# Performance work log

Measured on AMD Instinct MI355X. Metric: run time of the kernel, lower is better.

## Reference

```python
import jax, jax.numpy as jnp
import numpy as np

N_NODES = 100000
N_EDGES = 1600000
NUM_GRAPHS = 64
IN_CH, HID, NUM_CLASSES = 128, 64, 10


def _glorot(key, fan_in, fan_out):
    scale = jnp.sqrt(2.0 / (fan_in + fan_out)).astype(jnp.float32)
    return jax.random.normal(key, (fan_in, fan_out), jnp.float32) * scale


def setup_inputs() -> dict:
    key = jax.random.key(0)
    ks = jax.random.split(key, 7)
    x = jax.random.normal(ks[0], (N_NODES, IN_CH), jnp.float32)
    edge_index = jax.random.randint(ks[1], (2, N_EDGES), 0, N_NODES, dtype=jnp.int32)
    batch = jnp.sort(jax.random.randint(ks[2], (N_NODES,), 0, NUM_GRAPHS, dtype=jnp.int32))
    return {
        "x": x,
        "edge_index": edge_index,
        "batch": batch,
        "W1": _glorot(ks[3], IN_CH, HID), "b1": jnp.zeros((HID,), jnp.float32),
        "W2": _glorot(ks[4], HID, HID), "b2": jnp.zeros((HID,), jnp.float32),
        "W3": _glorot(ks[5], HID, NUM_CLASSES), "b3": jnp.zeros((NUM_CLASSES,), jnp.float32),
    }


def _gcn_conv(x, src, dst, norm, W, b):
    # GCNConv: h = X W, then symmetric-normalized scatter-add over edges, then + b
    h = x @ W                                  # [N, out]
    msg = norm[:, None] * h[src]               # [E+N, out] gather
    out = jax.ops.segment_sum(msg, dst, num_segments=N_NODES)
    return out + b


def reference(x, edge_index, batch, W1, b1, W2, b2, W3, b3):
    loop = jnp.arange(N_NODES, dtype=edge_index.dtype)
    src = jnp.concatenate([edge_index[0], loop])   # self-loops added (PyG gcn_norm)
    dst = jnp.concatenate([edge_index[1], loop])
    deg = jax.ops.segment_sum(jnp.ones(src.shape[0], x.dtype), dst, num_segments=N_NODES)
    dinv = jnp.where(deg > 0, jax.lax.rsqrt(deg), jnp.zeros_like(deg))
    norm = dinv[src] * dinv[dst]

    h = jax.nn.relu(_gcn_conv(x, src, dst, norm, W1, b1))  # dropout is identity in eval
    h = jax.nn.relu(_gcn_conv(h, src, dst, norm, W2, b2))
    h = _gcn_conv(h, src, dst, norm, W3, b3)

    counts = jax.ops.segment_sum(jnp.ones(N_NODES, h.dtype), batch, num_segments=NUM_GRAPHS)
    pooled = jax.ops.segment_sum(h, batch, num_segments=NUM_GRAPHS) / jnp.maximum(counts, 1.0)[:, None]
    return jax.nn.log_softmax(pooled, axis=1)
```

## Files before the change

kernel.cpp:

```cpp
#include <hip/hip_runtime.h>
#include <math.h>

#define IN_CH 128
#define HID   64
#define NC    10
#define BSH   8
#define NBLK  256

typedef unsigned short bfu;
typedef __attribute__((ext_vector_type(8))) short bf16x8;
typedef __attribute__((ext_vector_type(4))) float f32x4;
typedef __attribute__((ext_vector_type(2))) float f32x2;

static __device__ __forceinline__ bfu bf16_of(float f) {
    unsigned u = __float_as_uint(f);
    unsigned r = (u + 0x7FFF + ((u >> 16) & 1)) >> 16;
    return (bfu)r;
}

#if __has_builtin(__builtin_amdgcn_cvt_pk_f32_fp8) && __has_builtin(__builtin_amdgcn_cvt_pk_fp8_f32)
template <bool HI>
static __device__ __forceinline__ f32x2 fp8_unpk(unsigned d) {
    return __builtin_amdgcn_cvt_pk_f32_fp8((int)d, HI);
}
template <bool HI>
static __device__ __forceinline__ int fp8_pk(float a, float b, int old) {
    return __builtin_amdgcn_cvt_pk_fp8_f32(a, b, old, HI);
}
#else
static __device__ __forceinline__ float fp8_dec1(unsigned b) {
    unsigned s = b >> 7, e = (b >> 3) & 15, m = b & 7;
    float v = (e == 0) ? ldexpf((float)m, -9) : ldexpf((float)(8 + m), (int)e - 10);
    return s ? -v : v;
}
static __device__ __forceinline__ unsigned fp8_enc1(float f) {
    unsigned u = __float_as_uint(f);
    unsigned s = (u >> 31) << 7;
    f = fabsf(f);
    if (!(f < 448.f)) return s | 0x7E;
    if (f < 0.015625f) {
        int q = (int)rintf(f * 512.f);
        return s | (unsigned)q;
    }
    int e; float fr = frexpf(f, &e);
    int q = (int)rintf(fr * 16.f);
    if (q == 16) { q = 8; e++; }
    int E = e + 6;
    if (E >= 16) return s | 0x7E;
    return s | (unsigned)((E << 3) | (q - 8));
}
template <bool HI>
static __device__ __forceinline__ f32x2 fp8_unpk(unsigned d) {
    unsigned w = HI ? (d >> 16) : d;
    f32x2 r; r.x = fp8_dec1(w & 0xFF); r.y = fp8_dec1((w >> 8) & 0xFF);
    return r;
}
template <bool HI>
static __device__ __forceinline__ int fp8_pk(float a, float b, int old) {
    unsigned p = fp8_enc1(a) | (fp8_enc1(b) << 8);
    return HI ? (int)(((unsigned)old & 0x0000FFFFu) | (p << 16))
              : (int)(((unsigned)old & 0xFFFF0000u) | p);
}
#endif

__device__ __forceinline__ int lower_bound_i(const int* a, int n, int v) {
    int lo = 0, hi = n;
    while (lo < hi) { int mid = (lo + hi) >> 1; if (a[mid] < v) lo = mid + 1; else hi = mid; }
    return lo;
}


__global__ void k_init(int* __restrict__ cnt, float* __restrict__ Psum,
                       unsigned* __restrict__ dumA, unsigned* __restrict__ dumB,
                       int nbuck, int ng) {
    int t = threadIdx.x;
    for (int i = t; i < nbuck; i += 512) cnt[i] = 0;
    for (int i = t; i < ng * HID; i += 512) Psum[i] = 0.f;
    if (t < 16) { dumA[t] = 0u; dumB[t] = 0u; }
}


__global__ __launch_bounds__(1024) void k_part(const int* __restrict__ src,
                                               const int* __restrict__ dst,
                                               int* __restrict__ cnt,
                                               unsigned* __restrict__ packed,
                                               int E, int nbuck, int chunk, int cap) {
    __shared__ int hist[512];
    int tid = threadIdx.x;
    for (int b = tid; b < nbuck; b += 1024) hist[b] = 0;
    __syncthreads();
    int base = blockIdx.x * chunk;
    int lim  = min(base + chunk, E);
    for (int e = base + tid; e < lim; e += 1024)
        atomicAdd(&hist[dst[e] >> BSH], 1);
    __syncthreads();
    for (int b = tid; b < nbuck; b += 1024) {
        int c = hist[b];
        hist[b] = c ? atomicAdd(&cnt[b], c) : 0;
    }
    __syncthreads();
    for (int e = base + tid; e < lim; e += 1024) {
        int d = dst[e], s = src[e];
        int b = d >> BSH;
        int pos = atomicAdd(&hist[b], 1);
        if (pos < cap)
            packed[(size_t)b * (size_t)cap + pos] = ((unsigned)s << 8) | (unsigned)(d & 255);
    }
}


__global__ __launch_bounds__(512) void k_placeC(const unsigned* __restrict__ packed,
                                                const int* __restrict__ cnt,
                                                int2* __restrict__ rp2,
                                                float* __restrict__ dinv,
                                                int* __restrict__ meta,
                                                int nn, int cap, int capm) {
    __shared__ int hist[256];
    __shared__ int scn[256];
    __shared__ int cur[256];
    int tid = threadIdx.x;
    int b   = blockIdx.x;
    int nb0 = b << BSH;
    int nnb = min(1 << BSH, nn - nb0);
    if (tid < 256) hist[tid] = 0;
    __syncthreads();
    int lo = b * cap;
    int hi = lo + min(cnt[b], cap);
    for (int e = lo + tid; e < hi; e += blockDim.x)
        atomicAdd(&hist[packed[e] & 255u], 1);
    __syncthreads();
    int pd = 0;
    if (tid < 256) { pd = (hist[tid] + 3) & ~3; scn[tid] = pd; }
    __syncthreads();
    for (int off = 1; off < 256; off <<= 1) {
        int t = 0;
        if (tid < 256 && tid >= off) t = scn[tid - off];
        __syncthreads();
        if (tid < 256) scn[tid] += t;
        __syncthreads();
    }
    int meta0 = b * capm;
    if (tid < nnb) {
        int rp = meta0 + scn[tid] - pd;
        rp2[nb0 + tid] = make_int2(rp, rp + pd);
        cur[tid] = rp;
        dinv[nb0 + tid] = rsqrtf((float)(hist[tid] + 1));
        for (int k = hist[tid]; k < pd; k++) meta[rp + k] = nn;
    }
    __syncthreads();
    for (int e = lo + tid; e < hi; e += blockDim.x) {
        unsigned p = packed[e];
        int pos = atomicAdd(&cur[p & 255u], 1);
        meta[pos] = (int)(p >> 8);
    }
}


template <int K, bool IN_BF16>
__global__ __launch_bounds__(256) void k_gemm(const void* __restrict__ Xv,
                                              const float* __restrict__ W,
                                              const float* __restrict__ dinv,
                                              unsigned char* __restrict__ G8, int n) {
    constexpr int KS = K + 8;
    __shared__ bfu wt[64 * KS];
    int tid = threadIdx.x;
    for (int i = tid; i < K * 64; i += 256) {
        int k = i >> 6, nn2 = i & 63;
        wt[nn2 * KS + k] = bf16_of(W[i]);
    }
    __syncthreads();
    int wave = tid >> 6, lane = tid & 63;
    int m = lane & 15, q = lane >> 4;
    int row0 = blockIdx.x * 64 + wave * 16;
    int rowA = min(row0 + m, n - 1);
    f32x4 acc[4] = {{0.f,0.f,0.f,0.f},{0.f,0.f,0.f,0.f},
                    {0.f,0.f,0.f,0.f},{0.f,0.f,0.f,0.f}};
#pragma unroll
    for (int ks = 0; ks < K / 32; ks++) {
        bf16x8 a;
        if (IN_BF16) {
            a = *(const bf16x8*)((const bfu*)Xv + (size_t)rowA * 64 + ks * 32 + q * 8);
        } else {
            const float* xp = (const float*)Xv + (size_t)rowA * K + ks * 32 + q * 8;
            float4 v0 = *(const float4*)xp;
            float4 v1 = *(const float4*)(xp + 4);
            union { unsigned u[4]; bf16x8 v; } cvt;
            cvt.u[0] = __builtin_amdgcn_perm(__float_as_uint(v0.y), __float_as_uint(v0.x), 0x07060302u);
            cvt.u[1] = __builtin_amdgcn_perm(__float_as_uint(v0.w), __float_as_uint(v0.z), 0x07060302u);
            cvt.u[2] = __builtin_amdgcn_perm(__float_as_uint(v1.y), __float_as_uint(v1.x), 0x07060302u);
            cvt.u[3] = __builtin_amdgcn_perm(__float_as_uint(v1.w), __float_as_uint(v1.z), 0x07060302u);
            a = cvt.v;
        }
#pragma unroll
        for (int nt = 0; nt < 4; nt++) {
            bf16x8 b = *(const bf16x8*)&wt[(nt * 16 + m) * KS + ks * 32 + q * 8];
            acc[nt] = __builtin_amdgcn_mfma_f32_16x16x32_bf16(a, b, acc[nt], 0, 0, 0);
        }
    }
#pragma unroll
    for (int r = 0; r < 4; r++) {
        int grow = row0 + q * 4 + r;
        if (grow < n) {
            float dv = dinv[grow];
            int p01 = fp8_pk<false>(acc[0][r] * dv, acc[1][r] * dv, 0);
            int p23 = fp8_pk<false>(acc[2][r] * dv, acc[3][r] * dv, 0);
            unsigned char* gp = G8 + (size_t)grow * 64 + m;
            gp[0]  = (unsigned char)(p01 & 0xFF);
            gp[16] = (unsigned char)((p01 >> 8) & 0xFF);
            gp[32] = (unsigned char)(p23 & 0xFF);
            gp[48] = (unsigned char)((p23 >> 8) & 0xFF);
        }
    }
}


template <int MODE>
__global__ void k_agg(const unsigned* __restrict__ G4, const int* __restrict__ meta,
                      const int2* __restrict__ rp2, const float* __restrict__ dinv,
                      const float* __restrict__ bias, void* __restrict__ outv,
                      const int* __restrict__ batch, float* __restrict__ Psum,
                      const float* __restrict__ Wg,
                      int n, int ng, int do_relu, int post_scale) {
    extern __shared__ char smem[];
    int tid = threadIdx.x;
    if (MODE == 3) {
        bfu* wt = (bfu*)(smem + 16 * 72 * 2);
        for (int i = tid; i < 64 * 64; i += 256) {
            int k = i >> 6, c = i & 63;
            wt[c * 72 + k] = bf16_of(Wg[i]);
        }
    }
    int wbase = ((blockIdx.x * blockDim.x + tid) >> 6) * 4;
    if (MODE == 1) { if (wbase >= n) return; }
    int lane = tid & 63;
    int col4 = lane & 15, equad = lane >> 4;
    int nb0 = blockIdx.x * 16;
    if (MODE == 2 && tid < 16) {
        int* sb = (int*)(smem + 16 * 64 * 4);
        sb[tid] = (nb0 + tid < n) ? batch[nb0 + tid] : -1;
    }
    int nd    = wbase + equad;
    bool alive = nd < n;
    int ndc   = alive ? nd : (n - 1);
    int2 rp = rp2[ndc];
    int beg = rp.x, pend = alive ? rp.y : rp.x;
    f32x2 aA = {0.f, 0.f}, aB = {0.f, 0.f};
    for (int e = beg; e < pend; e += 4) {
        int4 m = *(const int4*)&meta[e];
        unsigned d0 = G4[(size_t)m.x * 16 + col4];
        unsigned d1 = G4[(size_t)m.y * 16 + col4];
        unsigned d2 = G4[(size_t)m.z * 16 + col4];
        unsigned d3 = G4[(size_t)m.w * 16 + col4];
        aA += fp8_unpk<false>(d0); aB += fp8_unpk<true>(d0);
        aA += fp8_unpk<false>(d1); aB += fp8_unpk<true>(d1);
        aA += fp8_unpk<false>(d2); aB += fp8_unpk<true>(d2);
        aA += fp8_unpk<false>(d3); aB += fp8_unpk<true>(d3);
    }
    unsigned sv = G4[(size_t)ndc * 16 + col4];
    aA += fp8_unpk<false>(sv); aB += fp8_unpk<true>(sv);
    float dv = dinv[ndc];
    float a0 = aA.x * dv, a1 = aA.y * dv, a2 = aB.x * dv, a3 = aB.y * dv;
    if (bias) {
        float4 bv = *(const float4*)&bias[col4 * 4];
        a0 += bv.x; a1 += bv.y; a2 += bv.z; a3 += bv.w;
    }
    if (do_relu) {
        a0 = fmaxf(a0, 0.f); a1 = fmaxf(a1, 0.f);
        a2 = fmaxf(a2, 0.f); a3 = fmaxf(a3, 0.f);
    }
    if (post_scale) { a0 *= dv; a1 *= dv; a2 *= dv; a3 *= dv; }
    if (MODE == 3) {
        bfu* pw = (bfu*)smem;
        bfu* wt = (bfu*)(smem + 16 * 72 * 2);
        int slot = (tid >> 6) * 4 + equad;
        uint2 o;
        o.x = (unsigned)bf16_of(alive ? a0 : 0.f) | ((unsigned)bf16_of(alive ? a1 : 0.f) << 16);
        o.y = (unsigned)bf16_of(alive ? a2 : 0.f) | ((unsigned)bf16_of(alive ? a3 : 0.f) << 16);
        *(uint2*)&pw[slot * 72 + col4 * 4] = o;
        __syncthreads();
        int w = tid >> 6, m = col4, q = equad;
        f32x4 acc = {0.f, 0.f, 0.f, 0.f};
#pragma unroll
        for (int ks = 0; ks < 2; ks++) {
            bf16x8 av = *(const bf16x8*)&pw[m * 72 + ks * 32 + q * 8];
            bf16x8 bv = *(const bf16x8*)&wt[(w * 16 + m) * 72 + ks * 32 + q * 8];
            acc = __builtin_amdgcn_mfma_f32_16x16x32_bf16(av, bv, acc, 0, 0, 0);
        }
        int c = w * 16 + m;
        int r0 = nb0 + q * 4;
        float dv0 = dinv[min(r0 + 0, n - 1)], dv1 = dinv[min(r0 + 1, n - 1)];
        float dv2 = dinv[min(r0 + 2, n - 1)], dv3 = dinv[min(r0 + 3, n - 1)];
        int p01 = fp8_pk<false>(acc[0] * dv0, acc[1] * dv1, 0);
        int p23 = fp8_pk<false>(acc[2] * dv2, acc[3] * dv3, 0);
        unsigned char* gp = (unsigned char*)outv;
        if (r0 + 0 < n) gp[(size_t)(r0 + 0) * 64 + c] = (unsigned char)(p01 & 0xFF);
        if (r0 + 1 < n) gp[(size_t)(r0 + 1) * 64 + c] = (unsigned char)((p01 >> 8) & 0xFF);
        if (r0 + 2 < n) gp[(size_t)(r0 + 2) * 64 + c] = (unsigned char)(p23 & 0xFF);
        if (r0 + 3 < n) gp[(size_t)(r0 + 3) * 64 + c] = (unsigned char)((p23 >> 8) & 0xFF);
    } else if (MODE == 2) {
        float* pwf = (float*)smem;
        int*   sb  = (int*)(smem + 16 * 64 * 4);
        int slot = (tid >> 6) * 4 + equad;
        f32x4 st;
        st.x = alive ? a0 : 0.f; st.y = alive ? a1 : 0.f;
        st.z = alive ? a2 : 0.f; st.w = alive ? a3 : 0.f;
        *(f32x4*)&pwf[slot * 64 + col4 * 4] = st;
        __syncthreads();
        int r = tid >> 6, cc = tid & 63;
        int g0 = sb[0];
        float v = 0.f;
#pragma unroll
        for (int s2 = 0; s2 < 16; s2++)
            if (sb[s2] == g0 + r) v += pwf[s2 * 64 + cc];
        if (v != 0.f && g0 + r < ng) atomicAdd(&Psum[(g0 + r) * 64 + cc], v);
        if (tid < 16) {
            int bb = sb[tid];
            if (bb > g0 + 3) {
                for (int c2 = 0; c2 < 64; c2++)
                    atomicAdd(&Psum[bb * 64 + c2], pwf[tid * 64 + c2]);
            }
        }
    } else if (alive) {
        int p = fp8_pk<false>(a0, a1, 0);
        p = fp8_pk<true>(a2, a3, p);
        ((unsigned*)outv)[(size_t)nd * 16 + col4] = (unsigned)p;
    }
}


__global__ void k_final(const float* __restrict__ Psum, const int* __restrict__ batch,
                        int n, const float* __restrict__ W3, const float* __restrict__ b3,
                        float* __restrict__ out, int ng) {
    __shared__ float P[64 * 64];
    __shared__ float s[64][NC];
    __shared__ float lse[64];
    __shared__ float invc[64];
    int t = threadIdx.x;
    if (t < ng) {
        int lo = lower_bound_i(batch, n, t);
        int hi = lower_bound_i(batch, n, t + 1);
        invc[t] = 1.f / (float)max(hi - lo, 1);
    }
    __syncthreads();
    for (int i = t; i < ng * 64; i += blockDim.x) P[i] = Psum[i] * invc[i >> 6];
    __syncthreads();
    if (t < ng * NC) {
        int g = t / NC, c = t % NC;
        float acc = b3[c];
        for (int k = 0; k < 64; k++) acc += P[g * 64 + k] * W3[k * NC + c];
        s[g][c] = acc;
    }
    __syncthreads();
    if (t < ng) {
        float m = -1e30f;
        for (int c = 0; c < NC; c++) m = fmaxf(m, s[t][c]);
        float sum = 0.f;
        for (int c = 0; c < NC; c++) sum += expf(s[t][c] - m);
        lse[t] = m + logf(sum);
    }
    __syncthreads();
    if (t < ng * NC) {
        int g = t / NC, c = t % NC;
        out[t] = s[g][c] - lse[g];
    }
}


extern "C" void kernel_launch(void* const* d_in, const int* in_sizes, int n_in,
                              void* d_out, int out_size, void* d_ws, size_t ws_size,
                              hipStream_t stream) {
    const float* x     = (const float*)d_in[0];
    const int*   ei    = (const int*)  d_in[1];
    const int*   batch = (const int*)  d_in[2];
    const float* W1    = (const float*)d_in[3];
    const float* b1    = (const float*)d_in[4];
    const float* W2    = (const float*)d_in[5];
    const float* b2    = (const float*)d_in[6];
    const float* W3    = (const float*)d_in[7];
    const float* b3    = (const float*)d_in[8];
    float*       out   = (float*)d_out;

    const int NN = in_sizes[0] / IN_CH;
    const int E  = in_sizes[1] / 2;
    const int NG = out_size / NC;
    const int nbuck = (NN + (1 << BSH) - 1) >> BSH;
    const int cap   = (int)(((((long long)E << BSH) / NN) + 768 + 3) & ~3LL);
    const int capm  = cap + 772;

    const int* src = ei;
    const int* dst = ei + E;

    char* ws = (char*)d_ws;
    size_t off = 0;
    auto carve = [&](size_t bytes) -> char* {
        char* p = ws + off;
        off = (off + bytes + 255) & ~(size_t)255;
        return p;
    };
    int2*  rp2    = (int2*) carve((size_t)NN * 8);
    float* dinv   = (float*)carve((size_t)NN * 4);
    int*   cnt    = (int*)  carve((size_t)nbuck * 4);
    int*   meta   = (int*)  carve(((size_t)nbuck * capm + 64) * 4);
    unsigned char* f8A = (unsigned char*)carve((size_t)(NN + 1) * 64);
    unsigned char* f8B = (unsigned char*)carve((size_t)(NN + 1) * 64);
    unsigned* packed = (unsigned*)carve((size_t)nbuck * cap * 4);
    float* Psum   = (float*)carve((size_t)NG * HID * 4);
    (void)ws_size;

    const int chnk = (E + NBLK - 1) / NBLK;
    const int nbG  = (NN + 63) / 64;
    const int nbA  = (NN + 15) / 16;

    const int smem3 = (16 * 72 + 64 * 72) * 2;
    const int smem2 = 16 * 64 * 4 + 16 * 4;

    k_init<<<1, 512, 0, stream>>>(cnt, Psum,
                                  (unsigned*)(f8A + (size_t)NN * 64),
                                  (unsigned*)(f8B + (size_t)NN * 64), nbuck, NG);
    k_part<<<NBLK, 1024, 0, stream>>>(src, dst, cnt, packed, E, nbuck, chnk, cap);
    k_placeC<<<nbuck, 512, 0, stream>>>(packed, cnt, rp2, dinv, meta, NN, cap, capm);

    k_gemm<IN_CH, false><<<nbG, 256, 0, stream>>>(x, W1, dinv, f8A, NN);
    k_agg<3><<<nbA, 256, smem3, stream>>>((const unsigned*)f8A, meta, rp2, dinv, b1,
                                          f8B, nullptr, nullptr, W2, NN, NG, 1, 0);
    k_agg<1><<<nbA, 256, 0, stream>>>((const unsigned*)f8B, meta, rp2, dinv, b2,
                                      f8A, nullptr, nullptr, nullptr, NN, NG, 1, 1);
    k_agg<2><<<nbA, 256, smem2, stream>>>((const unsigned*)f8A, meta, rp2, dinv, nullptr,
                                          nullptr, batch, Psum, nullptr, NN, NG, 0, 0);
    k_final<<<1, 640, 0, stream>>>(Psum, batch, NN, W3, b3, out, NG);
}
```

Before: 246.4 us.

## Pre-convert weights to bf16 once, unroll aggregation gather, widen placement blocks

Weights W1 and W2 are converted to transposed, padded bf16 once in a multi-block init kernel. The GEMM and layer-1 aggregation blocks then copy them into shared memory with 16-byte vector loads instead of each block converting fp32 again. The aggregation inner loop gathers 8 neighbours per iteration, and the self-feature and dinv loads are hoisted ahead of the loop to add memory-level parallelism. k_placeC now launches 1024 threads per block. This adds small workspace buffers and relies on the padded layouts matching the shared-memory strides exactly.

```diff
diff --git a/kernel.cpp b/kernel.cpp
--- a/kernel.cpp
+++ b/kernel.cpp
@@ -72,11 +72,30 @@
 
 __global__ void k_init(int* __restrict__ cnt, float* __restrict__ Psum,
                        unsigned* __restrict__ dumA, unsigned* __restrict__ dumB,
+                       const float* __restrict__ W1, const float* __restrict__ W2,
+                       bfu* __restrict__ W1b, bfu* __restrict__ W2b,
                        int nbuck, int ng) {
-    int t = threadIdx.x;
-    for (int i = t; i < nbuck; i += 512) cnt[i] = 0;
-    for (int i = t; i < ng * HID; i += 512) Psum[i] = 0.f;
-    if (t < 16) { dumA[t] = 0u; dumB[t] = 0u; }
+    int t = threadIdx.x, b = blockIdx.x;
+    if (b == 0) {
+        for (int i = t; i < nbuck; i += 256) cnt[i] = 0;
+        if (t < 16) { dumA[t] = 0u; dumB[t] = 0u; }
+    } else if (b == 1) {
+        for (int i = t; i < ng * HID; i += 256) Psum[i] = 0.f;
+    } else if (b < 6) {
+        int base = (b - 2) * 2048;
+        for (int i = t; i < 2048; i += 256) {
+            int idx = base + i;
+            int k = idx >> 6, c = idx & 63;
+            W1b[c * 136 + k] = bf16_of(W1[idx]);
+        }
+    } else {
+        int base = (b - 6) * 2048;
+        for (int i = t; i < 2048; i += 256) {
+            int idx = base + i;
+            int k = idx >> 6, c = idx & 63;
+            W2b[c * 72 + k] = bf16_of(W2[idx]);
+        }
+    }
 }
 
 
@@ -109,12 +128,12 @@
 }
 
 
-__global__ __launch_bounds__(512) void k_placeC(const unsigned* __restrict__ packed,
-                                                const int* __restrict__ cnt,
-                                                int2* __restrict__ rp2,
-                                                float* __restrict__ dinv,
-                                                int* __restrict__ meta,
-                                                int nn, int cap, int capm) {
+__global__ __launch_bounds__(1024) void k_placeC(const unsigned* __restrict__ packed,
+                                                 const int* __restrict__ cnt,
+                                                 int2* __restrict__ rp2,
+                                                 float* __restrict__ dinv,
+                                                 int* __restrict__ meta,
+                                                 int nn, int cap, int capm) {
     __shared__ int hist[256];
     __shared__ int scn[256];
     __shared__ int cur[256];
@@ -158,15 +177,16 @@
 
 template <int K, bool IN_BF16>
 __global__ __launch_bounds__(256) void k_gemm(const void* __restrict__ Xv,
-                                              const float* __restrict__ W,
+                                              const bfu* __restrict__ Wb,
                                               const float* __restrict__ dinv,
                                               unsigned char* __restrict__ G8, int n) {
     constexpr int KS = K + 8;
     __shared__ bfu wt[64 * KS];
     int tid = threadIdx.x;
-    for (int i = tid; i < K * 64; i += 256) {
-        int k = i >> 6, nn2 = i & 63;
-        wt[nn2 * KS + k] = bf16_of(W[i]);
+    {
+        const uint4* wsrc = (const uint4*)Wb;
+        uint4* wdst = (uint4*)wt;
+        for (int i = tid; i < 8 * KS; i += 256) wdst[i] = wsrc[i];
     }
     __syncthreads();
     int wave = tid >> 6, lane = tid & 63;
@@ -219,16 +239,15 @@
                       const int2* __restrict__ rp2, const float* __restrict__ dinv,
                       const float* __restrict__ bias, void* __restrict__ outv,
                       const int* __restrict__ batch, float* __restrict__ Psum,
-                      const float* __restrict__ Wg,
+                      const bfu* __restrict__ Wb,
                       int n, int ng, int do_relu, int post_scale) {
     extern __shared__ char smem[];
     int tid = threadIdx.x;
     if (MODE == 3) {
         bfu* wt = (bfu*)(smem + 16 * 72 * 2);
-        for (int i = tid; i < 64 * 64; i += 256) {
-            int k = i >> 6, c = i & 63;
-            wt[c * 72 + k] = bf16_of(Wg[i]);
-        }
+        const uint4* wsrc = (const uint4*)Wb;
+        uint4* wdst = (uint4*)wt;
+        for (int i = tid; i < 576; i += 256) wdst[i] = wsrc[i];
     }
     int wbase = ((blockIdx.x * blockDim.x + tid) >> 6) * 4;
     if (MODE == 1) { if (wbase >= n) return; }
@@ -244,8 +263,31 @@
     int ndc   = alive ? nd : (n - 1);
     int2 rp = rp2[ndc];
     int beg = rp.x, pend = alive ? rp.y : rp.x;
+    unsigned sv = G4[(size_t)ndc * 16 + col4];
+    float dv = dinv[ndc];
     f32x2 aA = {0.f, 0.f}, aB = {0.f, 0.f};
-    for (int e = beg; e < pend; e += 4) {
+    int e = beg;
+    for (; e + 8 <= pend; e += 8) {
+        int4 m0 = *(const int4*)&meta[e];
+        int4 m1 = *(const int4*)&meta[e + 4];
+        unsigned d0 = G4[(size_t)m0.x * 16 + col4];
+        unsigned d1 = G4[(size_t)m0.y * 16 + col4];
+        unsigned d2 = G4[(size_t)m0.z * 16 + col4];
+        unsigned d3 = G4[(size_t)m0.w * 16 + col4];
+        unsigned d4 = G4[(size_t)m1.x * 16 + col4];
+        unsigned d5 = G4[(size_t)m1.y * 16 + col4];
+        unsigned d6 = G4[(size_t)m1.z * 16 + col4];
+        unsigned d7 = G4[(size_t)m1.w * 16 + col4];
+        aA += fp8_unpk<false>(d0); aB += fp8_unpk<true>(d0);
+        aA += fp8_unpk<false>(d1); aB += fp8_unpk<true>(d1);
+        aA += fp8_unpk<false>(d2); aB += fp8_unpk<true>(d2);
+        aA += fp8_unpk<false>(d3); aB += fp8_unpk<true>(d3);
+        aA += fp8_unpk<false>(d4); aB += fp8_unpk<true>(d4);
+        aA += fp8_unpk<false>(d5); aB += fp8_unpk<true>(d5);
+        aA += fp8_unpk<false>(d6); aB += fp8_unpk<true>(d6);
+        aA += fp8_unpk<false>(d7); aB += fp8_unpk<true>(d7);
+    }
+    if (e < pend) {
         int4 m = *(const int4*)&meta[e];
         unsigned d0 = G4[(size_t)m.x * 16 + col4];
         unsigned d1 = G4[(size_t)m.y * 16 + col4];
@@ -256,9 +298,7 @@
         aA += fp8_unpk<false>(d2); aB += fp8_unpk<true>(d2);
         aA += fp8_unpk<false>(d3); aB += fp8_unpk<true>(d3);
     }
-    unsigned sv = G4[(size_t)ndc * 16 + col4];
     aA += fp8_unpk<false>(sv); aB += fp8_unpk<true>(sv);
-    float dv = dinv[ndc];
     float a0 = aA.x * dv, a1 = aA.y * dv, a2 = aB.x * dv, a3 = aB.y * dv;
     if (bias) {
         float4 bv = *(const float4*)&bias[col4 * 4];
@@ -405,6 +445,8 @@
     unsigned char* f8B = (unsigned char*)carve((size_t)(NN + 1) * 64);
     unsigned* packed = (unsigned*)carve((size_t)nbuck * cap * 4);
     float* Psum   = (float*)carve((size_t)NG * HID * 4);
+    bfu*   W1b    = (bfu*)  carve((size_t)64 * 136 * 2);
+    bfu*   W2b    = (bfu*)  carve((size_t)64 * 72 * 2);
     (void)ws_size;
 
     const int chnk = (E + NBLK - 1) / NBLK;
@@ -414,15 +456,16 @@
     const int smem3 = (16 * 72 + 64 * 72) * 2;
     const int smem2 = 16 * 64 * 4 + 16 * 4;
 
-    k_init<<<1, 512, 0, stream>>>(cnt, Psum,
+    k_init<<<8, 256, 0, stream>>>(cnt, Psum,
                                   (unsigned*)(f8A + (size_t)NN * 64),
-                                  (unsigned*)(f8B + (size_t)NN * 64), nbuck, NG);
+                                  (unsigned*)(f8B + (size_t)NN * 64),
+                                  W1, W2, W1b, W2b, nbuck, NG);
     k_part<<<NBLK, 1024, 0, stream>>>(src, dst, cnt, packed, E, nbuck, chnk, cap);
-    k_placeC<<<nbuck, 512, 0, stream>>>(packed, cnt, rp2, dinv, meta, NN, cap, capm);
-
-    k_gemm<IN_CH, false><<<nbG, 256, 0, stream>>>(x, W1, dinv, f8A, NN);
+    k_placeC<<<nbuck, 1024, 0, stream>>>(packed, cnt, rp2, dinv, meta, NN, cap, capm);
+
+    k_gemm<IN_CH, false><<<nbG, 256, 0, stream>>>(x, W1b, dinv, f8A, NN);
     k_agg<3><<<nbA, 256, smem3, stream>>>((const unsigned*)f8A, meta, rp2, dinv, b1,
-                                          f8B, nullptr, nullptr, W2, NN, NG, 1, 0);
+                                          f8B, nullptr, nullptr, W2b, NN, NG, 1, 0);
     k_agg<1><<<nbA, 256, 0, stream>>>((const unsigned*)f8B, meta, rp2, dinv, b2,
                                       f8A, nullptr, nullptr, nullptr, NN, NG, 1, 1);
     k_agg<2><<<nbA, 256, smem2, stream>>>((const unsigned*)f8A, meta, rp2, dinv, nullptr,
```

After: 232.5 us, median of 2. -5.6%, faster.
